# Performance work log

Hardware: AMD Instinct MI355X
Metric: run time of the kernel (lower is better)

## Reference

```python
import jax, jax.numpy as jnp
import numpy as np

N, F, E, K = 7650, 745, 238162, 3  # nodes, feats, edges, poly depth
A_J, B_J = 1.0, 1.0                # Jacobi polynomial (a, b)
L_DOM, R_DOM = -1.0, 1.0           # Jacobi domain [l, r]


def setup_inputs() -> dict:
    key = jax.random.key(0)
    ks = jax.random.split(key, 16)
    u = lambda k, s: jax.random.uniform(k, s, jnp.float32, -0.1, 0.1)
    return {
        "X": jax.random.normal(ks[0], (N, F), jnp.float32),
        "edge_index": jax.random.randint(ks[1], (2, E), 0, N, jnp.int32),
        "edge_attr": jnp.ones((E,), jnp.float32),
        "W1": jax.random.normal(ks[2], (F, F), jnp.float32) / np.float32(np.sqrt(F)),
        "b1": u(ks[3], (F,)),
        "W2": jax.random.normal(ks[4], (F, F), jnp.float32) / np.float32(np.sqrt(F)),
        "b2": u(ks[5], (F,)),
        "W3": jax.random.normal(ks[6], (F, F), jnp.float32) / np.float32(np.sqrt(F)),
        "b3": u(ks[7], (F,)),
        "alphas_raw": jnp.ones((K + 1,), jnp.float32),
        "core": u(ks[8], (8, 3, 3, 8)),
        "U0": u(ks[9], (N, 8)),
        "U1": u(ks[10], (F, 3)),
        "U2": u(ks[11], (3, 3)),
        "U3": u(ks[12], (8, 8)),
        "trl_bias": jnp.zeros((1,), jnp.float32),
    }


def _spmm(row, col, w, x):
    # y[i] = sum_{e: row[e]=i} w[e] * x[col[e]]   -- irregular gather/scatter
    return jax.ops.segment_sum(w[:, None] * x[col], row, num_segments=N)


def _jacobi_step(L, x_lm1, x_lm2, Ax_lm1, alphas):
    a, b, l, r = A_J, B_J, L_DOM, R_DOM
    if L == 1:
        coef1 = (a - b) / 2 - (a + b + 2) / 2 * (l + r) / (r - l)
        coef2 = (a + b + 2) / (r - l)
        return alphas[0] * (coef1 * x_lm1 + coef2 * Ax_lm1)
    coef_l = 2 * L * (L + a + b) * (2 * L - 2 + a + b)
    coef_lm1_1 = (2 * L + a + b - 1) * (2 * L + a + b) * (2 * L + a + b - 2)
    coef_lm1_2 = (2 * L + a + b - 1) * (a * a - b * b)
    coef_lm2 = 2 * (L - 1 + a) * (L - 1 + b) * (2 * L + a + b)
    tmp1 = alphas[L - 1] * (coef_lm1_1 / coef_l)
    tmp2 = alphas[L - 1] * (coef_lm1_2 / coef_l)
    tmp3 = alphas[L - 1] * alphas[L - 2] * (coef_lm2 / coef_l)
    tmp1_2 = tmp1 * (2.0 / (r - l))
    tmp2_2 = tmp1 * ((r + l) / (r - l)) + tmp2
    return tmp1_2 * Ax_lm1 - tmp2_2 * x_lm1 - tmp3 * x_lm2


def _poly_conv(x, row, col, w, alphas):
    xs = [x]
    for L in range(1, K + 1):  # fixed small depth, unrolled
        Ax = _spmm(row, col, w, xs[-1])
        prev2 = xs[-2] if L >= 2 else xs[-1]
        xs.append(_jacobi_step(L, xs[-1], prev2, Ax, alphas))
    out = xs[0]
    for t in xs[1:]:
        out = out + t
    return out


def reference(X, edge_index, edge_attr, W1, b1, W2, b2, W3, b3,
              alphas_raw, core, U0, U1, U2, U3, trl_bias):
    row, col = edge_index[0], edge_index[1]
    # GCN-normalized adjacency weights D^{-1/2} A D^{-1/2}
    deg = jax.ops.segment_sum(edge_attr, row, num_segments=N)
    dis = jnp.where(deg > 0, 1.0 / jnp.sqrt(jnp.maximum(deg, 1e-12)), 0.0)
    w = dis[row] * edge_attr * dis[col]
    alphas = jnp.tanh(alphas_raw)  # basealpha=1.0

    def layer(x, Wm, bm):
        return _poly_conv(x @ Wm + bm, row, col, w, alphas)

    zeros_in = jnp.zeros((N, F), X.dtype)
    t0 = layer(X, W1, b1)
    t1 = layer(zeros_in, W2, b2)  # faithful: source feeds still-zero slice
    t2 = layer(zeros_in, W3, b3)
    T = jnp.stack([t0, t1, t2], axis=-1)  # [N, F, 3]

    # W = core x_0 U0 x_1 U1 x_2 U2 x_3 U3 -- done in factored form (same math)
    t = jnp.einsum('nfc,nr->rfc', T, U0)
    t = jnp.einsum('rfc,fs->rsc', t, U1)
    t = jnp.einsum('rsc,ct->rst', t, U2)
    t = jnp.einsum('rst,rstu->u', t, core)
    out = jnp.einsum('u,ou->o', t, U3)[None, :] + trl_bias  # [1, 8]
    return jax.nn.log_softmax(out, axis=-1)
```

## Files before the change

### kernel.cpp

```cpp
#include <hip/hip_runtime.h>
#include <math.h>

constexpr int N_NODES = 7650;
constexpr int F_FEAT  = 745;
constexpr int E_EDGES = 238162;
constexpr int NC1     = F_FEAT * 3;
constexpr int PAD     = 128;

constexpr size_t OFF_CF    = 0;
constexpr size_t OFF_BU    = 16;
constexpr size_t OFF_C1    = 128;
constexpr size_t OFF_DEG   = 2432;
constexpr size_t OFF_CNT   = 10112;
constexpr size_t OFF_EPACK = 17792;
constexpr size_t OFF_B0    = 1976192;
constexpr size_t OFF_B1    = 2006912;
constexpr size_t OFF_B2    = 2037632;
constexpr size_t OFF_RPART = 2068352;

constexpr int BLD_BLOCKS  = 1024;
constexpr int BLD_THREADS = 512;
constexpr int SCAT_BLOCKS = 256;

constexpr int SPMM_TPB  = 256;
constexpr int SPMM_GRID = (N_NODES * 16 + SPMM_TPB - 1) / SPMM_TPB;

__device__ __forceinline__ void jacobi_coefs(const float* __restrict__ alphas_raw,
                                             float* __restrict__ cf) {
    float al[4];
    #pragma unroll
    for (int i = 0; i < 4; ++i) al[i] = tanhf(alphas_raw[i]);
    const float a = 1.f, b = 1.f, l = -1.f, r = 1.f;
    float coef1 = (a - b) * 0.5f - (a + b + 2.f) * 0.5f * (l + r) / (r - l);
    float coef2 = (a + b + 2.f) / (r - l);
    cf[0] = al[0] * coef2;
    cf[1] = -al[0] * coef1;
    cf[2] = 0.f;
    for (int L = 2; L <= 3; ++L) {
        float Lf = (float)L;
        float coef_l     = 2.f * Lf * (Lf + a + b) * (2.f * Lf - 2.f + a + b);
        float coef_lm1_1 = (2.f * Lf + a + b - 1.f) * (2.f * Lf + a + b) * (2.f * Lf + a + b - 2.f);
        float coef_lm1_2 = (2.f * Lf + a + b - 1.f) * (a * a - b * b);
        float coef_lm2   = 2.f * (Lf - 1.f + a) * (Lf - 1.f + b) * (2.f * Lf + a + b);
        float tmp1   = al[L - 1] * (coef_lm1_1 / coef_l);
        float tmp2   = al[L - 1] * (coef_lm1_2 / coef_l);
        float tmp3   = al[L - 1] * al[L - 2] * (coef_lm2 / coef_l);
        int o = 3 * (L - 1);
        cf[o + 0] = tmp1 * (2.f / (r - l));
        cf[o + 1] = tmp1 * ((r + l) / (r - l)) + tmp2;
        cf[o + 2] = tmp3;
    }
}

__device__ __forceinline__ float disv(float dg) {
    return (dg > 0.f) ? 1.f / sqrtf(fmaxf(dg, 1e-12f)) : 0.f;
}

constexpr int INIT_BLOCKS = 205;
__global__ void init_kernel(const float* __restrict__ alphas_raw, const float* __restrict__ b1,
                            const float* __restrict__ b2, const float* __restrict__ b3,
                            const float* __restrict__ U1, const float* __restrict__ W1,
                            float* __restrict__ ws) {
    int b = blockIdx.x, t = threadIdx.x;
    if (b < 8) {
        float* deg = ws + OFF_DEG;
        int*   cnt = (int*)(ws + OFF_CNT);
        for (int i = b * 256 + t; i < N_NODES; i += 8 * 256) { deg[i] = 0.f; cnt[i] = 0; }
        return;
    }
    if (b == 8) {
        if (t == 0) jacobi_coefs(alphas_raw, ws + OFF_CF);
        return;
    }
    if (b < 18) {
        if (t >= 64) return;
        int o = b - 9, j = o / 3, s = o - j * 3;
        const float* bb = (j == 0) ? b1 : ((j == 1) ? b2 : b3);
        float acc = 0.f;
        for (int k = t; k < F_FEAT; k += 64) acc += bb[k] * U1[k * 3 + s];
        #pragma unroll
        for (int off = 32; off; off >>= 1) acc += __shfl_down(acc, off);
        if (t == 0) (ws + OFF_BU)[o] = acc;
        return;
    }
    int f = (b - 18) * 4 + (t >> 6), lane = t & 63;
    if (f >= F_FEAT) return;
    const float* wr = W1 + (size_t)f * F_FEAT;
    float s0 = 0.f, s1 = 0.f, s2 = 0.f;
    for (int k = lane; k < F_FEAT; k += 64) {
        float wv = wr[k];
        s0 += wv * U1[k * 3 + 0];
        s1 += wv * U1[k * 3 + 1];
        s2 += wv * U1[k * 3 + 2];
    }
    #pragma unroll
    for (int off = 32; off; off >>= 1) {
        s0 += __shfl_down(s0, off);
        s1 += __shfl_down(s1, off);
        s2 += __shfl_down(s2, off);
    }
    if (lane == 0) {
        float* C1 = ws + OFF_C1;
        C1[f * 3] = s0; C1[f * 3 + 1] = s1; C1[f * 3 + 2] = s2;
    }
}

__global__ __launch_bounds__(BLD_THREADS)
void build_kernel(const int* __restrict__ edge_index, const float* __restrict__ edge_attr,
                  const float* __restrict__ X, float* __restrict__ ws) {
    __shared__ float sC[NC1];
    const int t = threadIdx.x, b = blockIdx.x;
    if (b < SCAT_BLOCKS) {
        const int* row = edge_index;
        const int* col = edge_index + E_EDGES;
        float* deg  = ws + OFF_DEG;
        int*   cnt  = (int*)(ws + OFF_CNT);
        int2*  epk  = (int2*)(ws + OFF_EPACK);
        for (int e = b * BLD_THREADS + t; e < E_EDGES; e += SCAT_BLOCKS * BLD_THREADS) {
            int r = row[e];
            float av = edge_attr[e];
            atomicAdd(&deg[r], av);
            int p = atomicAdd(&cnt[r], 1);
            if (p < PAD) epk[r * PAD + p] = make_int2(col[e], __float_as_int(av));
        }
        return;
    }
    const float* C1 = ws + OFF_C1;
    for (int i = t; i < NC1; i += BLD_THREADS) sC[i] = C1[i];
    __syncthreads();
    const int lane = t & 63;
    const int XW = (BLD_BLOCKS - SCAT_BLOCKS) * (BLD_THREADS / 64);
    int xw = (b - SCAT_BLOCKS) * (BLD_THREADS / 64) + (t >> 6);
    float4* B0 = (float4*)(ws + OFF_B0);
    for (int rowi = xw; rowi < N_NODES; rowi += XW) {
        const float* xr = X + (size_t)rowi * F_FEAT;
        float s0 = 0.f, s1 = 0.f, s2 = 0.f;
        for (int k = lane; k < F_FEAT; k += 64) {
            float xv = xr[k];
            s0 += xv * sC[k * 3 + 0];
            s1 += xv * sC[k * 3 + 1];
            s2 += xv * sC[k * 3 + 2];
        }
        #pragma unroll
        for (int off = 32; off; off >>= 1) {
            s0 += __shfl_down(s0, off);
            s1 += __shfl_down(s1, off);
            s2 += __shfl_down(s2, off);
        }
        if (lane == 0) B0[rowi] = make_float4(s0, s1, s2, 1.f);
    }
}

__global__ void spmm1_kernel(float* __restrict__ ws) {
    int gid = blockIdx.x * (SPMM_TPB >> 4) + (threadIdx.x >> 4);
    int sub = threadIdx.x & 15;
    if (gid >= N_NODES) return;
    const float* deg = ws + OFF_DEG;
    const int*   cnt = (const int*)(ws + OFF_CNT);
    int2*        epk = (int2*)(ws + OFF_EPACK);
    const float4* B0 = (const float4*)(ws + OFF_B0);
    float4*       B1 = (float4*)(ws + OFF_B1);
    const float* cf = ws + OFF_CF;

    int s = cnt[gid]; if (s > PAD) s = PAD;
    int base = gid * PAD;
    float ax = 0.f, ay = 0.f, az = 0.f, aw = 0.f;
    for (int j = sub; j < s; j += 16) {
        int2 pk = epk[base + j];
        int c = pk.x;
        float wv = __int_as_float(pk.y) * disv(deg[c]);
        epk[base + j] = make_int2(c, __float_as_int(wv));
        float4 v = B0[c];
        ax += wv * v.x; ay += wv * v.y; az += wv * v.z; aw += wv * v.w;
    }
    #pragma unroll
    for (int off = 8; off; off >>= 1) {
        ax += __shfl_xor(ax, off, 16); ay += __shfl_xor(ay, off, 16);
        az += __shfl_xor(az, off, 16); aw += __shfl_xor(aw, off, 16);
    }
    if (sub == 0) {
        float cA = cf[0] * disv(deg[gid]), cB = cf[1];
        float4 x1 = B0[gid];
        B1[gid] = make_float4(cA * ax - cB * x1.x, cA * ay - cB * x1.y,
                              cA * az - cB * x1.z, cA * aw - cB * x1.w);
    }
}

__global__ void spmm2_kernel(float* __restrict__ ws) {
    int gid = blockIdx.x * (SPMM_TPB >> 4) + (threadIdx.x >> 4);
    int sub = threadIdx.x & 15;
    if (gid >= N_NODES) return;
    const float* deg = ws + OFF_DEG;
    const int*   cnt = (const int*)(ws + OFF_CNT);
    const int2*  epk = (const int2*)(ws + OFF_EPACK);
    const float4* B0 = (const float4*)(ws + OFF_B0);
    const float4* B1 = (const float4*)(ws + OFF_B1);
    float4*       B2 = (float4*)(ws + OFF_B2);
    const float* cf = ws + OFF_CF + 3;

    int s = cnt[gid]; if (s > PAD) s = PAD;
    int base = gid * PAD;
    float ax = 0.f, ay = 0.f, az = 0.f, aw = 0.f;
    for (int j = sub; j < s; j += 16) {
        int2 pk = epk[base + j];
        float wv = __int_as_float(pk.y);
        float4 v = B1[pk.x];
        ax += wv * v.x; ay += wv * v.y; az += wv * v.z; aw += wv * v.w;
    }
    #pragma unroll
    for (int off = 8; off; off >>= 1) {
        ax += __shfl_xor(ax, off, 16); ay += __shfl_xor(ay, off, 16);
        az += __shfl_xor(az, off, 16); aw += __shfl_xor(aw, off, 16);
    }
    if (sub == 0) {
        float cA = cf[0] * disv(deg[gid]), cB = cf[1], cC = cf[2];
        float4 x1 = B1[gid], x2 = B0[gid];
        B2[gid] = make_float4(cA * ax - cB * x1.x - cC * x2.x,
                              cA * ay - cB * x1.y - cC * x2.y,
                              cA * az - cB * x1.z - cC * x2.z,
                              cA * aw - cB * x1.w - cC * x2.w);
    }
}

__global__ void spmm3_reduce_kernel(const float* __restrict__ U0, float* __restrict__ ws) {
    __shared__ float smem[544];
    const int t = threadIdx.x, b = blockIdx.x;
    int gid = b * (SPMM_TPB >> 4) + (t >> 4);
    int sub = t & 15;
    const float* deg = ws + OFF_DEG;
    const int*   cnt = (const int*)(ws + OFF_CNT);
    const int2*  epk = (const int2*)(ws + OFF_EPACK);
    const float4* B0 = (const float4*)(ws + OFF_B0);
    const float4* B1 = (const float4*)(ws + OFF_B1);
    const float4* B2 = (const float4*)(ws + OFF_B2);
    float* Rp = ws + OFF_RPART;
    const float* cf = ws + OFF_CF + 6;

    float4 racc = make_float4(0.f, 0.f, 0.f, 0.f);
    if (gid < N_NODES) {
        int s = cnt[gid]; if (s > PAD) s = PAD;
        int base = gid * PAD;
        float ax = 0.f, ay = 0.f, az = 0.f, aw = 0.f;
        for (int j = sub; j < s; j += 16) {
            int2 pk = epk[base + j];
            float wv = __int_as_float(pk.y);
            float4 v = B2[pk.x];
            ax += wv * v.x; ay += wv * v.y; az += wv * v.z; aw += wv * v.w;
        }
        #pragma unroll
        for (int off = 8; off; off >>= 1) {
            ax += __shfl_xor(ax, off, 16); ay += __shfl_xor(ay, off, 16);
            az += __shfl_xor(az, off, 16); aw += __shfl_xor(aw, off, 16);
        }
        float cA = cf[0] * disv(deg[gid]), cB = cf[1], cC = cf[2];
        float4 x1 = B2[gid], x2 = B1[gid], x0 = B0[gid];
        float4 b3 = make_float4(cA * ax - cB * x1.x - cC * x2.x,
                                cA * ay - cB * x1.y - cC * x2.y,
                                cA * az - cB * x1.z - cC * x2.z,
                                cA * aw - cB * x1.w - cC * x2.w);
        if (sub < 8) {
            float u = U0[(size_t)gid * 8 + sub];
            racc.x = u * (x0.x + x1.x + x2.x + b3.x);
            racc.y = u * (x0.y + x1.y + x2.y + b3.y);
            racc.z = u * (x0.z + x1.z + x2.z + b3.z);
            racc.w = u * (x0.w + x1.w + x2.w + b3.w);
        }
    }
    int g = t >> 4;
    if (sub < 8) {
        smem[g * 32 + sub * 4 + 0] = racc.x;
        smem[g * 32 + sub * 4 + 1] = racc.y;
        smem[g * 32 + sub * 4 + 2] = racc.z;
        smem[g * 32 + sub * 4 + 3] = racc.w;
    }
    __syncthreads();
    if (t < 32) {
        float tot = 0.f;
        #pragma unroll
        for (int k = 0; k < 16; ++k) tot += smem[k * 32 + t];
        Rp[b * 32 + t] = tot;
    }
}

__global__ void final_kernel(const float* __restrict__ U2, const float* __restrict__ core,
                             const float* __restrict__ U3, const float* __restrict__ trl_bias,
                             float* __restrict__ ws, float* __restrict__ out) {
    __shared__ float sCore[576];
    __shared__ float sU3[64];
    __shared__ float sU2[9];
    __shared__ float sBu[9];
    __shared__ float sR[32];
    __shared__ float sRst[72];
    __shared__ float sUvec[8];
    __shared__ float sO[8];
    __shared__ float sred[256];
    __shared__ float sBias;
    const int t = threadIdx.x;
    const float* Rp = ws + OFF_RPART;
    const float* bu = ws + OFF_BU;

    for (int i = t; i < 576; i += 256) sCore[i] = core[i];
    if (t < 64) sU3[t] = U3[t];
    if (t >= 64 && t < 73) sU2[t - 64] = U2[t - 64];
    if (t >= 96 && t < 105) sBu[t - 96] = bu[t - 96];
    if (t == 128) sBias = trl_bias[0];

    float p = 0.f;
    for (int b2 = t >> 5; b2 < SPMM_GRID; b2 += 8) p += Rp[b2 * 32 + (t & 31)];
    sred[t] = p;
    __syncthreads();
    if (t < 32) {
        float tot = 0.f;
        #pragma unroll
        for (int k = 0; k < 8; ++k) tot += sred[k * 32 + t];
        sR[t] = tot;
    }
    __syncthreads();

    if (t < 72) {
        int rr = t / 9, rem = t - rr * 9, s = rem / 3, tt = rem - s * 3;
        float q  = sR[rr * 4 + 3];
        float m0 = sR[rr * 4 + s] + q * sBu[s];
        float m1 = q * sBu[3 + s];
        float m2 = q * sBu[6 + s];
        sRst[t] = m0 * sU2[tt] + m1 * sU2[3 + tt] + m2 * sU2[6 + tt];
    }
    __syncthreads();

    if (t < 8) {
        float acc = 0.f;
        #pragma unroll 8
        for (int k = 0; k < 72; ++k) acc += sRst[k] * sCore[k * 8 + t];
        sUvec[t] = acc;
    }
    __syncthreads();

    if (t < 8) {
        float acc = sBias;
        #pragma unroll
        for (int u = 0; u < 8; ++u) acc += sUvec[u] * sU3[t * 8 + u];
        sO[t] = acc;
    }
    __syncthreads();

    if (t == 0) {
        float mx = -1e30f;
        #pragma unroll
        for (int k = 0; k < 8; ++k) mx = fmaxf(mx, sO[k]);
        float se = 0.f;
        #pragma unroll
        for (int k = 0; k < 8; ++k) se += expf(sO[k] - mx);
        float lse = mx + logf(se);
        #pragma unroll
        for (int k = 0; k < 8; ++k) out[k] = sO[k] - lse;
    }
}

extern "C" void kernel_launch(void* const* d_in, const int* in_sizes, int n_in,
                              void* d_out, int out_size, void* d_ws, size_t ws_size,
                              hipStream_t stream) {
    const float* X          = (const float*)d_in[0];
    const int*   edge_index = (const int*)d_in[1];
    const float* edge_attr  = (const float*)d_in[2];
    const float* W1         = (const float*)d_in[3];
    const float* b1         = (const float*)d_in[4];
    const float* b2         = (const float*)d_in[6];
    const float* b3         = (const float*)d_in[8];
    const float* alphas_raw = (const float*)d_in[9];
    const float* core       = (const float*)d_in[10];
    const float* U0         = (const float*)d_in[11];
    const float* U1         = (const float*)d_in[12];
    const float* U2         = (const float*)d_in[13];
    const float* U3         = (const float*)d_in[14];
    const float* trl_bias   = (const float*)d_in[15];

    float* ws   = (float*)d_ws;
    float* outp = (float*)d_out;

    init_kernel<<<INIT_BLOCKS, 256, 0, stream>>>(alphas_raw, b1, b2, b3, U1, W1, ws);
    build_kernel<<<BLD_BLOCKS, BLD_THREADS, 0, stream>>>(edge_index, edge_attr, X, ws);
    spmm1_kernel<<<SPMM_GRID, SPMM_TPB, 0, stream>>>(ws);
    spmm2_kernel<<<SPMM_GRID, SPMM_TPB, 0, stream>>>(ws);
    spmm3_reduce_kernel<<<SPMM_GRID, SPMM_TPB, 0, stream>>>(U0, ws);
    final_kernel<<<1, 256, 0, stream>>>(U2, core, U3, trl_bias, ws, outp);
}
```

Baseline: 74.55 us.

## Split build into scatter, projection and degree kernels; precompute inverse-sqrt degree

Replaces the fused build kernel with three kernels. A one-edge-per-thread scatter drops the float degree atomic. An X-projection kernel uses one wave per row. A segmented degree kernel sums edge weights from the packed CSR and stores D^-1/2 once. The SpMM kernels then read the precomputed dis instead of recomputing sqrt per edge. This removes an atomic per edge and the repeated sqrt, but adds two launches and serialises the scatter and the projection, which previously ran concurrently.

```diff
diff --git a/kernel.cpp b/kernel.cpp
--- a/kernel.cpp
+++ b/kernel.cpp
@@ -10,7 +10,7 @@
 constexpr size_t OFF_CF    = 0;
 constexpr size_t OFF_BU    = 16;
 constexpr size_t OFF_C1    = 128;
-constexpr size_t OFF_DEG   = 2432;
+constexpr size_t OFF_DIS   = 2432;
 constexpr size_t OFF_CNT   = 10112;
 constexpr size_t OFF_EPACK = 17792;
 constexpr size_t OFF_B0    = 1976192;
@@ -18,9 +18,10 @@
 constexpr size_t OFF_B2    = 2037632;
 constexpr size_t OFF_RPART = 2068352;
 
-constexpr int BLD_BLOCKS  = 1024;
-constexpr int BLD_THREADS = 512;
-constexpr int SCAT_BLOCKS = 256;
+constexpr int SCT_THREADS = 512;
+constexpr int SCT_BLOCKS  = (E_EDGES + SCT_THREADS - 1) / SCT_THREADS;
+constexpr int XZ_THREADS  = 512;
+constexpr int XZ_BLOCKS   = (N_NODES + 7) / 8;
 
 constexpr int SPMM_TPB  = 256;
 constexpr int SPMM_GRID = (N_NODES * 16 + SPMM_TPB - 1) / SPMM_TPB;
@@ -63,9 +64,8 @@
                             float* __restrict__ ws) {
     int b = blockIdx.x, t = threadIdx.x;
     if (b < 8) {
-        float* deg = ws + OFF_DEG;
-        int*   cnt = (int*)(ws + OFF_CNT);
-        for (int i = b * 256 + t; i < N_NODES; i += 8 * 256) { deg[i] = 0.f; cnt[i] = 0; }
+        int* cnt = (int*)(ws + OFF_CNT);
+        for (int i = b * 256 + t; i < N_NODES; i += 8 * 256) cnt[i] = 0;
         return;
     }
     if (b == 8) {
@@ -105,57 +105,69 @@
     }
 }
 
-__global__ __launch_bounds__(BLD_THREADS)
-void build_kernel(const int* __restrict__ edge_index, const float* __restrict__ edge_attr,
-                  const float* __restrict__ X, float* __restrict__ ws) {
+__global__ __launch_bounds__(SCT_THREADS)
+void scatter_kernel(const int* __restrict__ edge_index, const float* __restrict__ edge_attr,
+                    float* __restrict__ ws) {
+    int e = blockIdx.x * SCT_THREADS + threadIdx.x;
+    if (e >= E_EDGES) return;
+    const int* row = edge_index;
+    const int* col = edge_index + E_EDGES;
+    int*  cnt = (int*)(ws + OFF_CNT);
+    int2* epk = (int2*)(ws + OFF_EPACK);
+    int r    = row[e];
+    int c    = col[e];
+    float av = edge_attr[e];
+    int p = atomicAdd(&cnt[r], 1);
+    if (p < PAD) epk[r * PAD + p] = make_int2(c, __float_as_int(av));
+}
+
+__global__ __launch_bounds__(XZ_THREADS)
+void xz_kernel(const float* __restrict__ X, float* __restrict__ ws) {
     __shared__ float sC[NC1];
-    const int t = threadIdx.x, b = blockIdx.x;
-    if (b < SCAT_BLOCKS) {
-        const int* row = edge_index;
-        const int* col = edge_index + E_EDGES;
-        float* deg  = ws + OFF_DEG;
-        int*   cnt  = (int*)(ws + OFF_CNT);
-        int2*  epk  = (int2*)(ws + OFF_EPACK);
-        for (int e = b * BLD_THREADS + t; e < E_EDGES; e += SCAT_BLOCKS * BLD_THREADS) {
-            int r = row[e];
-            float av = edge_attr[e];
-            atomicAdd(&deg[r], av);
-            int p = atomicAdd(&cnt[r], 1);
-            if (p < PAD) epk[r * PAD + p] = make_int2(col[e], __float_as_int(av));
-        }
-        return;
-    }
+    const int t = threadIdx.x;
     const float* C1 = ws + OFF_C1;
-    for (int i = t; i < NC1; i += BLD_THREADS) sC[i] = C1[i];
+    for (int i = t; i < NC1; i += XZ_THREADS) sC[i] = C1[i];
     __syncthreads();
     const int lane = t & 63;
-    const int XW = (BLD_BLOCKS - SCAT_BLOCKS) * (BLD_THREADS / 64);
-    int xw = (b - SCAT_BLOCKS) * (BLD_THREADS / 64) + (t >> 6);
-    float4* B0 = (float4*)(ws + OFF_B0);
-    for (int rowi = xw; rowi < N_NODES; rowi += XW) {
-        const float* xr = X + (size_t)rowi * F_FEAT;
-        float s0 = 0.f, s1 = 0.f, s2 = 0.f;
-        for (int k = lane; k < F_FEAT; k += 64) {
-            float xv = xr[k];
-            s0 += xv * sC[k * 3 + 0];
-            s1 += xv * sC[k * 3 + 1];
-            s2 += xv * sC[k * 3 + 2];
-        }
-        #pragma unroll
-        for (int off = 32; off; off >>= 1) {
-            s0 += __shfl_down(s0, off);
-            s1 += __shfl_down(s1, off);
-            s2 += __shfl_down(s2, off);
-        }
-        if (lane == 0) B0[rowi] = make_float4(s0, s1, s2, 1.f);
-    }
+    int rowi = blockIdx.x * (XZ_THREADS / 64) + (t >> 6);
+    if (rowi >= N_NODES) return;
+    const float* xr = X + (size_t)rowi * F_FEAT;
+    float s0 = 0.f, s1 = 0.f, s2 = 0.f;
+    for (int k = lane; k < F_FEAT; k += 64) {
+        float xv = xr[k];
+        s0 += xv * sC[k * 3 + 0];
+        s1 += xv * sC[k * 3 + 1];
+        s2 += xv * sC[k * 3 + 2];
+    }
+    #pragma unroll
+    for (int off = 32; off; off >>= 1) {
+        s0 += __shfl_down(s0, off);
+        s1 += __shfl_down(s1, off);
+        s2 += __shfl_down(s2, off);
+    }
+    if (lane == 0) ((float4*)(ws + OFF_B0))[rowi] = make_float4(s0, s1, s2, 1.f);
+}
+
+__global__ void deg_kernel(float* __restrict__ ws) {
+    int gid = blockIdx.x * (SPMM_TPB >> 4) + (threadIdx.x >> 4);
+    int sub = threadIdx.x & 15;
+    if (gid >= N_NODES) return;
+    const int*  cnt = (const int*)(ws + OFF_CNT);
+    const int2* epk = (const int2*)(ws + OFF_EPACK);
+    int s = cnt[gid]; if (s > PAD) s = PAD;
+    int base = gid * PAD;
+    float dg = 0.f;
+    for (int j = sub; j < s; j += 16) dg += __int_as_float(epk[base + j].y);
+    #pragma unroll
+    for (int off = 8; off; off >>= 1) dg += __shfl_xor(dg, off, 16);
+    if (sub == 0) (ws + OFF_DIS)[gid] = disv(dg);
 }
 
 __global__ void spmm1_kernel(float* __restrict__ ws) {
     int gid = blockIdx.x * (SPMM_TPB >> 4) + (threadIdx.x >> 4);
     int sub = threadIdx.x & 15;
     if (gid >= N_NODES) return;
-    const float* deg = ws + OFF_DEG;
+    const float* dis = ws + OFF_DIS;
     const int*   cnt = (const int*)(ws + OFF_CNT);
     int2*        epk = (int2*)(ws + OFF_EPACK);
     const float4* B0 = (const float4*)(ws + OFF_B0);
@@ -168,7 +180,7 @@
     for (int j = sub; j < s; j += 16) {
         int2 pk = epk[base + j];
         int c = pk.x;
-        float wv = __int_as_float(pk.y) * disv(deg[c]);
+        float wv = __int_as_float(pk.y) * dis[c];
         epk[base + j] = make_int2(c, __float_as_int(wv));
         float4 v = B0[c];
         ax += wv * v.x; ay += wv * v.y; az += wv * v.z; aw += wv * v.w;
@@ -179,7 +191,7 @@
         az += __shfl_xor(az, off, 16); aw += __shfl_xor(aw, off, 16);
     }
     if (sub == 0) {
-        float cA = cf[0] * disv(deg[gid]), cB = cf[1];
+        float cA = cf[0] * dis[gid], cB = cf[1];
         float4 x1 = B0[gid];
         B1[gid] = make_float4(cA * ax - cB * x1.x, cA * ay - cB * x1.y,
                               cA * az - cB * x1.z, cA * aw - cB * x1.w);
@@ -190,7 +202,7 @@
     int gid = blockIdx.x * (SPMM_TPB >> 4) + (threadIdx.x >> 4);
     int sub = threadIdx.x & 15;
     if (gid >= N_NODES) return;
-    const float* deg = ws + OFF_DEG;
+    const float* dis = ws + OFF_DIS;
     const int*   cnt = (const int*)(ws + OFF_CNT);
     const int2*  epk = (const int2*)(ws + OFF_EPACK);
     const float4* B0 = (const float4*)(ws + OFF_B0);
@@ -213,7 +225,7 @@
         az += __shfl_xor(az, off, 16); aw += __shfl_xor(aw, off, 16);
     }
     if (sub == 0) {
-        float cA = cf[0] * disv(deg[gid]), cB = cf[1], cC = cf[2];
+        float cA = cf[0] * dis[gid], cB = cf[1], cC = cf[2];
         float4 x1 = B1[gid], x2 = B0[gid];
         B2[gid] = make_float4(cA * ax - cB * x1.x - cC * x2.x,
                               cA * ay - cB * x1.y - cC * x2.y,
@@ -227,7 +239,7 @@
     const int t = threadIdx.x, b = blockIdx.x;
     int gid = b * (SPMM_TPB >> 4) + (t >> 4);
     int sub = t & 15;
-    const float* deg = ws + OFF_DEG;
+    const float* dis = ws + OFF_DIS;
     const int*   cnt = (const int*)(ws + OFF_CNT);
     const int2*  epk = (const int2*)(ws + OFF_EPACK);
     const float4* B0 = (const float4*)(ws + OFF_B0);
@@ -252,7 +264,7 @@
             ax += __shfl_xor(ax, off, 16); ay += __shfl_xor(ay, off, 16);
             az += __shfl_xor(az, off, 16); aw += __shfl_xor(aw, off, 16);
         }
-        float cA = cf[0] * disv(deg[gid]), cB = cf[1], cC = cf[2];
+        float cA = cf[0] * dis[gid], cB = cf[1], cC = cf[2];
         float4 x1 = B2[gid], x2 = B1[gid], x0 = B0[gid];
         float4 b3 = make_float4(cA * ax - cB * x1.x - cC * x2.x,
                                 cA * ay - cB * x1.y - cC * x2.y,
@@ -378,7 +390,9 @@
     float* outp = (float*)d_out;
 
     init_kernel<<<INIT_BLOCKS, 256, 0, stream>>>(alphas_raw, b1, b2, b3, U1, W1, ws);
-    build_kernel<<<BLD_BLOCKS, BLD_THREADS, 0, stream>>>(edge_index, edge_attr, X, ws);
+    scatter_kernel<<<SCT_BLOCKS, SCT_THREADS, 0, stream>>>(edge_index, edge_attr, ws);
+    xz_kernel<<<XZ_BLOCKS, XZ_THREADS, 0, stream>>>(X, ws);
+    deg_kernel<<<SPMM_GRID, SPMM_TPB, 0, stream>>>(ws);
     spmm1_kernel<<<SPMM_GRID, SPMM_TPB, 0, stream>>>(ws);
     spmm2_kernel<<<SPMM_GRID, SPMM_TPB, 0, stream>>>(ws);
     spmm3_reduce_kernel<<<SPMM_GRID, SPMM_TPB, 0, stream>>>(U0, ws);
```

New measurement: 65.58 us. 12.0% less time.
